# Kernel tuning notes

Hardware: AMD Instinct MI355X
Metric: run time of the kernel (lower is better)

## Reference

```python
import jax, jax.numpy as jnp
import numpy as np

T, N, D, H = 128, 64, 512, 512

def setup_inputs() -> dict:
    key = jax.random.key(0)
    ks = jax.random.split(key, 8)
    x = jax.random.normal(ks[0], (T * N, D), jnp.float32)
    hxs = jax.random.normal(ks[1], (N, H), jnp.float32)
    hxs_1 = jax.random.normal(ks[2], (N, H), jnp.float32)
    masks = jax.random.randint(ks[3], (T * N, 1), 0, 2).astype(jnp.float32)
    w_ih = jax.random.normal(ks[4], (3 * H, D), jnp.float32) / np.sqrt(D).astype(np.float32)
    w_hh = jax.random.normal(ks[5], (3 * H, H), jnp.float32) / np.sqrt(H).astype(np.float32)
    b_ih = jnp.zeros((3 * H,), jnp.float32)
    b_hh = jnp.zeros((3 * H,), jnp.float32)
    return {"x": x, "hxs": hxs, "hxs_1": hxs_1, "masks": masks,
            "w_ih": w_ih, "w_hh": w_hh, "b_ih": b_ih, "b_hh": b_hh}


def _masked_gru(x, hxs, masks, w_ih, w_hh, b_ih, b_hh):
    # Fused equivalent of the torch segment-splitting loop: the torch code
    # resets the hidden state (h * mask) at every step where any mask is 0;
    # within a segment all masks are 1, so applying h * mask_t every step is
    # exactly equivalent, with no host sync / dynamic splitting.
    n = hxs.shape[0]
    h_dim = hxs.shape[1]
    t = x.shape[0] // n
    xt = x.reshape(t, n, -1)            # [T, N, D]
    mt = masks.reshape(t, n, 1)         # [T, N, 1]
    # Precompute all input projections in one big GEMM: [T, N, 3H]
    gi = jnp.einsum('tnd,gd->tng', xt, w_ih) + b_ih

    def step(h, inp):
        gi_t, m_t = inp
        h = h * m_t                      # per-step mask reset
        gh = h @ w_hh.T + b_hh           # [N, 3H]
        i_r, i_z, i_n = jnp.split(gi_t, 3, axis=-1)
        h_r, h_z, h_n = jnp.split(gh, 3, axis=-1)
        r = jax.nn.sigmoid(i_r + h_r)
        z = jax.nn.sigmoid(i_z + h_z)
        ncand = jnp.tanh(i_n + r * h_n)
        h_new = (1.0 - z) * ncand + z * h
        return h_new, h_new

    h_last, outs = jax.lax.scan(step, hxs, (gi, mt))
    return outs.reshape(t * n, h_dim), h_last


def reference(x, hxs, hxs_1, masks, w_ih, w_hh, b_ih, b_hh):
    out, h_last = _masked_gru(x, hxs, masks, w_ih, w_hh, b_ih, b_hh)
    return out, h_last, hxs_1
```

## Files before the change

kernel.cpp:

```cpp
#include <hip/hip_runtime.h>
#include <cmath>

#define TT 128
#define NN 64
#define DD 512
#define HH 512
#define GG 1536

#define META_OFF   0
#define BATCH_OFF  1024
#define TASK_OFF   32768
#define WT_OFF     262144
#define GI_OFF     4194304
#define WS_NEEDED  (GI_OFF + (size_t)TT * NN * GG * 4)

__global__ void build_tasks(const float* __restrict__ masks,
                            int* __restrict__ meta,
                            int4* __restrict__ tasks,
                            int4* __restrict__ batches) {
  __shared__ int hist[TT + 1];
  __shared__ int offs[TT + 1];
  const int tid = threadIdx.x;
  for (int i = tid; i <= TT; i += blockDim.x) hist[i] = 0;
  __syncthreads();
  if (tid < NN) {
    const int n = tid;
    int start = 0;
    for (int t = 1; t < TT; ++t) {
      if (masks[t * NN + n] == 0.0f) { atomicAdd(&hist[t - start], 1); start = t; }
    }
    atomicAdd(&hist[TT - start], 1);
  }
  __syncthreads();
  if (tid == 0) {
    int acc = 0;
    for (int l = TT; l >= 1; --l) { offs[l] = acc; acc += hist[l]; }
    meta[0] = acc;
  }
  __syncthreads();
  const int totalTasks = meta[0];
  if (tid < NN) {
    const int n = tid;
    int start = 0;
    for (int t = 1; t < TT; ++t) {
      if (masks[t * NN + n] == 0.0f) {
        const int len = t - start;
        const int pos = atomicAdd(&offs[len], 1);
        const int seeded = (start == 0 && masks[n] != 0.0f) ? 1 : 0;
        tasks[pos] = make_int4(n, start, len, seeded);
        start = t;
      }
    }
    const int len = TT - start;
    const int pos = atomicAdd(&offs[len], 1);
    const int seeded = (start == 0 && masks[n] != 0.0f) ? 1 : 0;
    tasks[pos] = make_int4(n, start, len, seeded);
  }
  __syncthreads();
  if (tid == 0) {
    const int c0end = offs[5];
    const int c1end = offs[3];
    int b = 0;
    for (int p = 0; p < c0end; p += 4) {
      int c = c0end - p; if (c > 4) c = 4;
      batches[b++] = make_int4(p, 4, c, 0);
    }
    for (int p = c0end; p < c1end; p += 8) {
      int c = c1end - p; if (c > 8) c = 8;
      batches[b++] = make_int4(p, 8, c, 0);
    }
    for (int p = c1end; p < totalTasks; p += 16) {
      int c = totalTasks - p; if (c > 16) c = 16;
      batches[b++] = make_int4(p, 16, c, 0);
    }
    meta[2] = b;
    meta[1] = 0;
  }
}

__global__ void transpose_whh(const float* __restrict__ w, float* __restrict__ wT) {
  const int k = blockIdx.y;
  const int r = blockIdx.x * 256 + threadIdx.x;
  wT[k * GG + r] = w[r * DD + k];
}

__global__ __launch_bounds__(256, 4) void gemm_gi(const float* __restrict__ x,
                                                  const float* __restrict__ w,
                                                  const float* __restrict__ bias,
                                                  float* __restrict__ gi) {
  __shared__ __align__(16) float As[32][132];
  __shared__ __align__(16) float Bs[32][132];
  const int tid = threadIdx.x;
  const int m0 = blockIdx.y * 128;
  const int n0 = blockIdx.x * 128;
  const int tx = tid & 15;
  const int ty = tid >> 4;
  float acc[8][8] = {};
  for (int k0 = 0; k0 < DD; k0 += 32) {
#pragma unroll
    for (int i = 0; i < 4; ++i) {
      const int q = tid + i * 256;
      const int row = q >> 3;
      const int kf = (q & 7) << 2;
      const float4 va = *(const float4*)&x[(size_t)(m0 + row) * DD + k0 + kf];
      As[kf + 0][row] = va.x; As[kf + 1][row] = va.y;
      As[kf + 2][row] = va.z; As[kf + 3][row] = va.w;
      const float4 vb = *(const float4*)&w[(size_t)(n0 + row) * DD + k0 + kf];
      Bs[kf + 0][row] = vb.x; Bs[kf + 1][row] = vb.y;
      Bs[kf + 2][row] = vb.z; Bs[kf + 3][row] = vb.w;
    }
    __syncthreads();
#pragma unroll
    for (int k = 0; k < 32; ++k) {
      float a[8], b[8];
      ((float4*)a)[0] = *(const float4*)&As[k][ty * 8];
      ((float4*)a)[1] = *(const float4*)&As[k][ty * 8 + 4];
      ((float4*)b)[0] = *(const float4*)&Bs[k][tx * 8];
      ((float4*)b)[1] = *(const float4*)&Bs[k][tx * 8 + 4];
#pragma unroll
      for (int i = 0; i < 8; ++i)
#pragma unroll
        for (int j = 0; j < 8; ++j) acc[i][j] = fmaf(a[i], b[j], acc[i][j]);
    }
    __syncthreads();
  }
  float bs[8];
  ((float4*)bs)[0] = *(const float4*)&bias[n0 + tx * 8];
  ((float4*)bs)[1] = *(const float4*)&bias[n0 + tx * 8 + 4];
#pragma unroll
  for (int i = 0; i < 8; ++i) {
    const int row = m0 + ty * 8 + i;
    float4 o0 = make_float4(acc[i][0] + bs[0], acc[i][1] + bs[1],
                            acc[i][2] + bs[2], acc[i][3] + bs[3]);
    float4 o1 = make_float4(acc[i][4] + bs[4], acc[i][5] + bs[5],
                            acc[i][6] + bs[6], acc[i][7] + bs[7]);
    *(float4*)&gi[(size_t)row * GG + n0 + tx * 8] = o0;
    *(float4*)&gi[(size_t)row * GG + n0 + tx * 8 + 4] = o1;
  }
}

template <int W>
__device__ __forceinline__ void process_batch(
    const float* __restrict__ gi, const float* __restrict__ wT,
    const float* __restrict__ hxs, const float* __restrict__ masks,
    float* __restrict__ out, float (*Hs)[16], const int4* s_task, int tid,
    float bh_r, float bh_z, float bh_n) {
  int t_n[W], t_t0[W], t_len[W];
  bool anySeed = false;
#pragma unroll
  for (int c = 0; c < W; ++c) {
    const int4 tk = s_task[c];
    t_n[c] = tk.x; t_t0[c] = tk.y; t_len[c] = tk.z;
    anySeed |= (tk.w != 0 && tk.z > 0);
  }
  const int maxlen = t_len[0];
#pragma unroll
  for (int c = 0; c < W; ++c) {
    float h0 = 0.0f;
    if (s_task[c].w != 0) h0 = masks[t_n[c]] * hxs[t_n[c] * HH + tid];
    Hs[tid][c] = h0;
  }
  __syncthreads();
  for (int s = 0; s < maxlen; ++s) {
    float accr[W], accz[W], accn[W];
#pragma unroll
    for (int c = 0; c < W; ++c) { accr[c] = 0.f; accz[c] = 0.f; accn[c] = 0.f; }
    if (s > 0 || anySeed) {
      const float* w = wT + tid;
#pragma unroll 4
      for (int k = 0; k < HH; ++k) {
        const float wr = w[0];
        const float wz = w[512];
        const float wn = w[1024];
        float hk[W];
        if constexpr (W >= 4)  ((float4*)hk)[0] = *(const float4*)&Hs[k][0];
        if constexpr (W >= 8)  ((float4*)hk)[1] = *(const float4*)&Hs[k][4];
        if constexpr (W >= 16) {
          ((float4*)hk)[2] = *(const float4*)&Hs[k][8];
          ((float4*)hk)[3] = *(const float4*)&Hs[k][12];
        }
#pragma unroll
        for (int c = 0; c < W; ++c) {
          accr[c] = fmaf(wr, hk[c], accr[c]);
          accz[c] = fmaf(wz, hk[c], accz[c]);
          accn[c] = fmaf(wn, hk[c], accn[c]);
        }
        w += GG;
      }
    }
    __syncthreads();
#pragma unroll
    for (int c = 0; c < W; ++c) {
      if (s < t_len[c]) {
        const int row = (t_t0[c] + s) * NN + t_n[c];
        const float* g = gi + (size_t)row * GG + tid;
        const float gr = g[0], gz = g[512], gn = g[1024];
        const float r = 1.0f / (1.0f + expf(-(gr + accr[c] + bh_r)));
        const float z = 1.0f / (1.0f + expf(-(gz + accz[c] + bh_z)));
        const float hold = Hs[tid][c];
        const float nc = tanhf(gn + r * (accn[c] + bh_n));
        const float hnew = (1.0f - z) * nc + z * hold;
        out[(size_t)row * HH + tid] = hnew;
        Hs[tid][c] = hnew;
      }
    }
    __syncthreads();
  }
}

__global__ __launch_bounds__(512, 2) void gru_seq(
    const float* __restrict__ gi, const float* __restrict__ wT,
    const float* __restrict__ b_hh, const float* __restrict__ hxs,
    const float* __restrict__ masks, float* __restrict__ out,
    int* __restrict__ meta, const int4* __restrict__ tasks,
    const int4* __restrict__ batches) {
  __shared__ __align__(16) float Hs[HH][16];
  __shared__ int4 s_task[16];
  __shared__ int s_bidx;
  const int tid = threadIdx.x;
  const float bh_r = b_hh[tid];
  const float bh_z = b_hh[512 + tid];
  const float bh_n = b_hh[1024 + tid];
  const int nBatches = meta[2];
  while (true) {
    if (tid == 0) s_bidx = atomicAdd(&meta[1], 1);
    __syncthreads();
    const int bidx = s_bidx;
    if (bidx >= nBatches) break;
    const int4 bd = batches[bidx];
    if (tid < 16) s_task[tid] = (tid < bd.z) ? tasks[bd.x + tid] : make_int4(0, 0, 0, 0);
    __syncthreads();
    switch (bd.y) {
      case 4:
        process_batch<4>(gi, wT, hxs, masks, out, Hs, s_task, tid, bh_r, bh_z, bh_n);
        break;
      case 8:
        process_batch<8>(gi, wT, hxs, masks, out, Hs, s_task, tid, bh_r, bh_z, bh_n);
        break;
      default:
        process_batch<16>(gi, wT, hxs, masks, out, Hs, s_task, tid, bh_r, bh_z, bh_n);
        break;
    }
  }
}

__global__ void tail_copy(const float4* __restrict__ src_out,
                          const float4* __restrict__ hxs1,
                          float4* __restrict__ dst) {
  const int i = blockIdx.x * 256 + threadIdx.x;
  if (i < 8192)
    dst[1048576 + i] = src_out[1040384 + i];
  else
    dst[1048576 + i] = hxs1[i - 8192];
}

extern "C" void kernel_launch(void* const* d_in, const int* in_sizes, int n_in,
                              void* d_out, int out_size, void* d_ws, size_t ws_size,
                              hipStream_t stream) {
  const float* x      = (const float*)d_in[0];
  const float* hxs    = (const float*)d_in[1];
  const float* hxs_1  = (const float*)d_in[2];
  const float* masks  = (const float*)d_in[3];
  const float* w_ih   = (const float*)d_in[4];
  const float* w_hh   = (const float*)d_in[5];
  const float* b_ih   = (const float*)d_in[6];
  const float* b_hh   = (const float*)d_in[7];
  float* out = (float*)d_out;
  char* ws = (char*)d_ws;
  if (ws_size < WS_NEEDED) return;

  int*  meta    = (int*)(ws + META_OFF);
  int4* batches = (int4*)(ws + BATCH_OFF);
  int4* tasks   = (int4*)(ws + TASK_OFF);
  float* wT     = (float*)(ws + WT_OFF);
  float* gi     = (float*)(ws + GI_OFF);

  build_tasks<<<1, 128, 0, stream>>>(masks, meta, tasks, batches);
  transpose_whh<<<dim3(6, 512), 256, 0, stream>>>(w_hh, wT);
  gemm_gi<<<dim3(12, 64), 256, 0, stream>>>(x, w_ih, b_ih, gi);
  gru_seq<<<256, 512, 0, stream>>>(gi, wT, b_hh, hxs, masks, out, meta, tasks, batches);
  tail_copy<<<64, 256, 0, stream>>>((const float4*)out, (const float4*)hxs_1,
                                    (float4*)out);
}
```

Baseline: 770.6 us.

## Replace per-segment sequential GRU with cooperative depth-round scheduling across the grid

Drops the segment-batch scheduler, in which each block ran whole segments sequentially and reread the transposed W_hh from global memory at every step. Rows are now grouped by depth since the last mask reset. One cooperative kernel processes each depth round across all 256 blocks, with each block holding a 16-column slice of W_hh in shared memory, and grid.sync runs between rounds. Rows where the mask is zero are computed up front without the recurrent matmul. The transpose and tail-copy kernels are folded in, at the cost of one grid-wide barrier per round and a launch that depends on cooperative residency.

```diff
diff --git a/kernel.cpp b/kernel.cpp
--- a/kernel.cpp
+++ b/kernel.cpp
@@ -1,5 +1,8 @@
 #include <hip/hip_runtime.h>
+#include <hip/hip_cooperative_groups.h>
 #include <cmath>
+
+namespace cg = cooperative_groups;
 
 #define TT 128
 #define NN 64
@@ -8,80 +11,67 @@
 #define GG 1536
 
 #define META_OFF   0
-#define BATCH_OFF  1024
-#define TASK_OFF   32768
-#define WT_OFF     262144
-#define GI_OFF     4194304
+#define ROFF_OFF   256
+#define ZROWS_OFF  4096
+#define ROWOUT_OFF 36864
+#define ROWHS_OFF  69632
+#define GI_OFF     1048576
 #define WS_NEEDED  (GI_OFF + (size_t)TT * NN * GG * 4)
 
-__global__ void build_tasks(const float* __restrict__ masks,
-                            int* __restrict__ meta,
-                            int4* __restrict__ tasks,
-                            int4* __restrict__ batches) {
-  __shared__ int hist[TT + 1];
-  __shared__ int offs[TT + 1];
+__global__ void build_rounds(const float* __restrict__ masks, int* __restrict__ meta,
+                             int* __restrict__ roundOff, int* __restrict__ zRows,
+                             int* __restrict__ rowOut, int* __restrict__ rowHsrc) {
+  __shared__ int cnt[129];
+  __shared__ int cur[129];
+  __shared__ int zcur;
   const int tid = threadIdx.x;
-  for (int i = tid; i <= TT; i += blockDim.x) hist[i] = 0;
+  for (int i = tid; i < 129; i += 128) cnt[i] = 0;
+  if (tid == 0) zcur = 0;
   __syncthreads();
   if (tid < NN) {
     const int n = tid;
-    int start = 0;
-    for (int t = 1; t < TT; ++t) {
-      if (masks[t * NN + n] == 0.0f) { atomicAdd(&hist[t - start], 1); start = t; }
-    }
-    atomicAdd(&hist[TT - start], 1);
+    int depth = 0;
+    for (int t = 0; t < TT; ++t) {
+      if (masks[t * NN + n] == 0.0f) {
+        depth = 0;
+        atomicAdd(&zcur, 1);
+      } else {
+        depth = (t == 0) ? 0 : depth + 1;
+        atomicAdd(&cnt[depth], 1);
+      }
+    }
   }
   __syncthreads();
   if (tid == 0) {
-    int acc = 0;
-    for (int l = TT; l >= 1; --l) { offs[l] = acc; acc += hist[l]; }
-    meta[0] = acc;
+    int acc = 0, maxs = -1;
+    for (int s = 0; s < 129; ++s) {
+      roundOff[s] = acc;
+      cur[s] = acc;
+      if (cnt[s] > 0) maxs = s;
+      acc += cnt[s];
+    }
+    roundOff[129] = acc;
+    meta[0] = maxs;
+    meta[1] = zcur;
+    zcur = 0;
   }
   __syncthreads();
-  const int totalTasks = meta[0];
   if (tid < NN) {
     const int n = tid;
-    int start = 0;
-    for (int t = 1; t < TT; ++t) {
+    int depth = 0;
+    for (int t = 0; t < TT; ++t) {
       if (masks[t * NN + n] == 0.0f) {
-        const int len = t - start;
-        const int pos = atomicAdd(&offs[len], 1);
-        const int seeded = (start == 0 && masks[n] != 0.0f) ? 1 : 0;
-        tasks[pos] = make_int4(n, start, len, seeded);
-        start = t;
-      }
-    }
-    const int len = TT - start;
-    const int pos = atomicAdd(&offs[len], 1);
-    const int seeded = (start == 0 && masks[n] != 0.0f) ? 1 : 0;
-    tasks[pos] = make_int4(n, start, len, seeded);
-  }
-  __syncthreads();
-  if (tid == 0) {
-    const int c0end = offs[5];
-    const int c1end = offs[3];
-    int b = 0;
-    for (int p = 0; p < c0end; p += 4) {
-      int c = c0end - p; if (c > 4) c = 4;
-      batches[b++] = make_int4(p, 4, c, 0);
-    }
-    for (int p = c0end; p < c1end; p += 8) {
-      int c = c1end - p; if (c > 8) c = 8;
-      batches[b++] = make_int4(p, 8, c, 0);
-    }
-    for (int p = c1end; p < totalTasks; p += 16) {
-      int c = totalTasks - p; if (c > 16) c = 16;
-      batches[b++] = make_int4(p, 16, c, 0);
-    }
-    meta[2] = b;
-    meta[1] = 0;
-  }
-}
-
-__global__ void transpose_whh(const float* __restrict__ w, float* __restrict__ wT) {
-  const int k = blockIdx.y;
-  const int r = blockIdx.x * 256 + threadIdx.x;
-  wT[k * GG + r] = w[r * DD + k];
+        depth = 0;
+        const int p = atomicAdd(&zcur, 1);
+        zRows[p] = t * NN + n;
+      } else {
+        depth = (t == 0) ? 0 : depth + 1;
+        const int p = atomicAdd(&cur[depth], 1);
+        rowOut[p] = t * NN + n;
+        rowHsrc[p] = (t == 0) ? (8192 + n) : ((t - 1) * NN + n);
+      }
+    }
+  }
 }
 
 __global__ __launch_bounds__(256, 4) void gemm_gi(const float* __restrict__ x,
@@ -139,146 +129,207 @@
   }
 }
 
-template <int W>
-__device__ __forceinline__ void process_batch(
-    const float* __restrict__ gi, const float* __restrict__ wT,
-    const float* __restrict__ hxs, const float* __restrict__ masks,
-    float* __restrict__ out, float (*Hs)[16], const int4* s_task, int tid,
-    float bh_r, float bh_z, float bh_n) {
-  int t_n[W], t_t0[W], t_len[W];
-  bool anySeed = false;
-#pragma unroll
-  for (int c = 0; c < W; ++c) {
-    const int4 tk = s_task[c];
-    t_n[c] = tk.x; t_t0[c] = tk.y; t_len[c] = tk.z;
-    anySeed |= (tk.w != 0 && tk.z > 0);
-  }
-  const int maxlen = t_len[0];
-#pragma unroll
-  for (int c = 0; c < W; ++c) {
-    float h0 = 0.0f;
-    if (s_task[c].w != 0) h0 = masks[t_n[c]] * hxs[t_n[c] * HH + tid];
-    Hs[tid][c] = h0;
-  }
+#define NGC 32
+#define GCW 16
+#define NRG 8
+#define RT  128
+#define KT  32
+#define WSTR 516
+#define HSTR 36
+
+__global__ __launch_bounds__(512) void gru_rounds(
+    const float* __restrict__ gi, const float* __restrict__ w_hh,
+    const float* __restrict__ b_hh, const float* __restrict__ hxs,
+    const float* __restrict__ hxs_1, float* __restrict__ out,
+    const int* __restrict__ meta, const int* __restrict__ roundOff,
+    const int* __restrict__ zRows, const int* __restrict__ rowOut,
+    const int* __restrict__ rowHsrc) {
+  __shared__ __align__(16) float wS[3 * GCW * WSTR];
+  __shared__ __align__(16) float hS[2 * RT * HSTR];
+  __shared__ const float* s_hbase[RT];
+  __shared__ int s_orow[RT];
+
+  const int tid = threadIdx.x;
+  const int bid = blockIdx.x;
+  const int cgrp = bid & (NGC - 1);
+  const int rg = bid >> 5;
+  const int wv = tid >> 6;
+  const int ln = tid & 63;
+  const int tc = ln & 15;
+  const int rsub = ln >> 4;
+  const int lrbase = wv * 16 + rsub * 4;
+  const int col = cgrp * GCW + tc;
+
+  {
+    const float* src = w_hh;
+    for (int q = tid; q < 3 * GCW * 128; q += 512) {
+      const int gr = q >> 7;
+      const int p = q & 127;
+      const int g = gr >> 4, r = gr & 15;
+      const float4 v =
+          *(const float4*)&src[((size_t)(g * 512 + cgrp * GCW + r)) * 512 + p * 4];
+      *(float4*)&wS[(g * GCW + r) * WSTR + p * 4] = v;
+    }
+  }
+  const float bhr = b_hh[col], bhz = b_hh[512 + col], bhn = b_hh[1024 + col];
   __syncthreads();
-  for (int s = 0; s < maxlen; ++s) {
-    float accr[W], accz[W], accn[W];
-#pragma unroll
-    for (int c = 0; c < W; ++c) { accr[c] = 0.f; accz[c] = 0.f; accn[c] = 0.f; }
-    if (s > 0 || anySeed) {
-      const float* w = wT + tid;
-#pragma unroll 4
-      for (int k = 0; k < HH; ++k) {
-        const float wr = w[0];
-        const float wz = w[512];
-        const float wn = w[1024];
-        float hk[W];
-        if constexpr (W >= 4)  ((float4*)hk)[0] = *(const float4*)&Hs[k][0];
-        if constexpr (W >= 8)  ((float4*)hk)[1] = *(const float4*)&Hs[k][4];
-        if constexpr (W >= 16) {
-          ((float4*)hk)[2] = *(const float4*)&Hs[k][8];
-          ((float4*)hk)[3] = *(const float4*)&Hs[k][12];
-        }
-#pragma unroll
-        for (int c = 0; c < W; ++c) {
-          accr[c] = fmaf(wr, hk[c], accr[c]);
-          accz[c] = fmaf(wz, hk[c], accz[c]);
-          accn[c] = fmaf(wn, hk[c], accn[c]);
-        }
-        w += GG;
-      }
-    }
-    __syncthreads();
-#pragma unroll
-    for (int c = 0; c < W; ++c) {
-      if (s < t_len[c]) {
-        const int row = (t_t0[c] + s) * NN + t_n[c];
-        const float* g = gi + (size_t)row * GG + tid;
-        const float gr = g[0], gz = g[512], gn = g[1024];
-        const float r = 1.0f / (1.0f + expf(-(gr + accr[c] + bh_r)));
-        const float z = 1.0f / (1.0f + expf(-(gz + accz[c] + bh_z)));
-        const float hold = Hs[tid][c];
-        const float nc = tanhf(gn + r * (accn[c] + bh_n));
-        const float hnew = (1.0f - z) * nc + z * hold;
-        out[(size_t)row * HH + tid] = hnew;
-        Hs[tid][c] = hnew;
-      }
-    }
-    __syncthreads();
-  }
-}
-
-__global__ __launch_bounds__(512, 2) void gru_seq(
-    const float* __restrict__ gi, const float* __restrict__ wT,
-    const float* __restrict__ b_hh, const float* __restrict__ hxs,
-    const float* __restrict__ masks, float* __restrict__ out,
-    int* __restrict__ meta, const int4* __restrict__ tasks,
-    const int4* __restrict__ batches) {
-  __shared__ __align__(16) float Hs[HH][16];
-  __shared__ int4 s_task[16];
-  __shared__ int s_bidx;
-  const int tid = threadIdx.x;
-  const float bh_r = b_hh[tid];
-  const float bh_z = b_hh[512 + tid];
-  const float bh_n = b_hh[1024 + tid];
-  const int nBatches = meta[2];
-  while (true) {
-    if (tid == 0) s_bidx = atomicAdd(&meta[1], 1);
-    __syncthreads();
-    const int bidx = s_bidx;
-    if (bidx >= nBatches) break;
-    const int4 bd = batches[bidx];
-    if (tid < 16) s_task[tid] = (tid < bd.z) ? tasks[bd.x + tid] : make_int4(0, 0, 0, 0);
-    __syncthreads();
-    switch (bd.y) {
-      case 4:
-        process_batch<4>(gi, wT, hxs, masks, out, Hs, s_task, tid, bh_r, bh_z, bh_n);
-        break;
-      case 8:
-        process_batch<8>(gi, wT, hxs, masks, out, Hs, s_task, tid, bh_r, bh_z, bh_n);
-        break;
-      default:
-        process_batch<16>(gi, wT, hxs, masks, out, Hs, s_task, tid, bh_r, bh_z, bh_n);
-        break;
-    }
-  }
-}
-
-__global__ void tail_copy(const float4* __restrict__ src_out,
-                          const float4* __restrict__ hxs1,
-                          float4* __restrict__ dst) {
-  const int i = blockIdx.x * 256 + threadIdx.x;
-  if (i < 8192)
-    dst[1048576 + i] = src_out[1040384 + i];
-  else
-    dst[1048576 + i] = hxs1[i - 8192];
+
+  cg::grid_group grid = cg::this_grid();
+  const int gtid = bid * 512 + tid;
+  const int gnt = gridDim.x * 512;
+
+  const int zcount = meta[1];
+  for (int idx = gtid; idx < zcount * 512; idx += gnt) {
+    const int zr = zRows[idx >> 9];
+    const int c = idx & 511;
+    const float* g = gi + (size_t)zr * GG + c;
+    const float r = 1.0f / (1.0f + expf(-(g[0] + b_hh[c])));
+    const float z = 1.0f / (1.0f + expf(-(g[512] + b_hh[512 + c])));
+    const float nc = tanhf(g[1024] + r * b_hh[1024 + c]);
+    out[(size_t)zr * HH + c] = (1.0f - z) * nc;
+  }
+
+  const int maxs = meta[0];
+  for (int s = 0; s <= maxs; ++s) {
+    const int base = roundOff[s];
+    const int cnt = roundOff[s + 1] - base;
+    const int chunk = (cnt + NRG - 1) / NRG;
+    const int rowStart = rg * chunk;
+    int myCnt = cnt - rowStart;
+    myCnt = myCnt < 0 ? 0 : (myCnt > chunk ? chunk : myCnt);
+
+    for (int t0 = 0; t0 < myCnt; t0 += RT) {
+      const int rows = min(RT, myCnt - t0);
+      __syncthreads();
+      for (int r = tid; r < RT; r += 512) {
+        if (r < rows) {
+          const int gidx = base + rowStart + t0 + r;
+          s_orow[r] = rowOut[gidx];
+          const int hs = rowHsrc[gidx];
+          s_hbase[r] = (hs >= 8192) ? (hxs + (size_t)(hs - 8192) * HH)
+                                    : (out + (size_t)hs * HH);
+        } else {
+          s_orow[r] = -1;
+          s_hbase[r] = hxs;
+        }
+      }
+      __syncthreads();
+
+      float acc[4][3];
+#pragma unroll
+      for (int j = 0; j < 4; ++j)
+#pragma unroll
+        for (int g2 = 0; g2 < 3; ++g2) acc[j][g2] = 0.0f;
+
+      const int sr0 = tid >> 3, sk0 = (tid & 7) * 4;
+      const int sr1 = (tid + 512) >> 3, sk1 = ((tid + 512) & 7) * 4;
+      float4 st0, st1;
+      st0 = *(const float4*)(s_hbase[sr0] + sk0);
+      st1 = *(const float4*)(s_hbase[sr1] + sk1);
+      *(float4*)&hS[sr0 * HSTR + sk0] = st0;
+      *(float4*)&hS[sr1 * HSTR + sk1] = st1;
+      st0 = *(const float4*)(s_hbase[sr0] + KT + sk0);
+      st1 = *(const float4*)(s_hbase[sr1] + KT + sk1);
+      __syncthreads();
+
+      const bool rowAct = (lrbase < rows);
+      for (int c = 0; c < 16; ++c) {
+        if (rowAct) {
+          const float* hbuf = hS + (c & 1) * RT * HSTR + lrbase * HSTR;
+          const float* wbuf = wS + tc * WSTR + c * KT;
+#pragma unroll
+          for (int kk = 0; kk < KT; kk += 4) {
+            const float4 w0 = *(const float4*)(wbuf + kk);
+            const float4 w1 = *(const float4*)(wbuf + GCW * WSTR + kk);
+            const float4 w2 = *(const float4*)(wbuf + 2 * GCW * WSTR + kk);
+#pragma unroll
+            for (int j = 0; j < 4; ++j) {
+              const float4 hv = *(const float4*)(hbuf + j * HSTR + kk);
+              acc[j][0] = fmaf(w0.x, hv.x, acc[j][0]);
+              acc[j][0] = fmaf(w0.y, hv.y, acc[j][0]);
+              acc[j][0] = fmaf(w0.z, hv.z, acc[j][0]);
+              acc[j][0] = fmaf(w0.w, hv.w, acc[j][0]);
+              acc[j][1] = fmaf(w1.x, hv.x, acc[j][1]);
+              acc[j][1] = fmaf(w1.y, hv.y, acc[j][1]);
+              acc[j][1] = fmaf(w1.z, hv.z, acc[j][1]);
+              acc[j][1] = fmaf(w1.w, hv.w, acc[j][1]);
+              acc[j][2] = fmaf(w2.x, hv.x, acc[j][2]);
+              acc[j][2] = fmaf(w2.y, hv.y, acc[j][2]);
+              acc[j][2] = fmaf(w2.z, hv.z, acc[j][2]);
+              acc[j][2] = fmaf(w2.w, hv.w, acc[j][2]);
+            }
+          }
+        }
+        if (c + 1 < 16) {
+          float* hb = hS + ((c + 1) & 1) * RT * HSTR;
+          *(float4*)&hb[sr0 * HSTR + sk0] = st0;
+          *(float4*)&hb[sr1 * HSTR + sk1] = st1;
+        }
+        if (c + 2 < 16) {
+          st0 = *(const float4*)(s_hbase[sr0] + (c + 2) * KT + sk0);
+          st1 = *(const float4*)(s_hbase[sr1] + (c + 2) * KT + sk1);
+        }
+        __syncthreads();
+      }
+
+#pragma unroll
+      for (int j = 0; j < 4; ++j) {
+        const int lr = lrbase + j;
+        if (lr < rows) {
+          const int orow = s_orow[lr];
+          const float* gp = gi + (size_t)orow * GG + col;
+          const float gr = gp[0], gz = gp[512], gn = gp[1024];
+          const float r = 1.0f / (1.0f + expf(-(gr + acc[j][0] + bhr)));
+          const float z = 1.0f / (1.0f + expf(-(gz + acc[j][1] + bhz)));
+          const float hold = s_hbase[lr][col];
+          const float nc = tanhf(gn + r * (acc[j][2] + bhn));
+          out[(size_t)orow * HH + col] = (1.0f - z) * nc + z * hold;
+        }
+      }
+    }
+    __threadfence();
+    grid.sync();
+  }
+
+  for (int i = gtid; i < 16384; i += gnt) {
+    float4 v;
+    if (i < 8192)
+      v = ((const float4*)out)[1040384 + i];
+    else
+      v = ((const float4*)hxs_1)[i - 8192];
+    ((float4*)out)[1048576 + i] = v;
+  }
 }
 
 extern "C" void kernel_launch(void* const* d_in, const int* in_sizes, int n_in,
                               void* d_out, int out_size, void* d_ws, size_t ws_size,
                               hipStream_t stream) {
-  const float* x      = (const float*)d_in[0];
-  const float* hxs    = (const float*)d_in[1];
-  const float* hxs_1  = (const float*)d_in[2];
-  const float* masks  = (const float*)d_in[3];
-  const float* w_ih   = (const float*)d_in[4];
-  const float* w_hh   = (const float*)d_in[5];
-  const float* b_ih   = (const float*)d_in[6];
-  const float* b_hh   = (const float*)d_in[7];
+  const float* x     = (const float*)d_in[0];
+  const float* hxs   = (const float*)d_in[1];
+  const float* hxs_1 = (const float*)d_in[2];
+  const float* masks = (const float*)d_in[3];
+  const float* w_ih  = (const float*)d_in[4];
+  const float* w_hh  = (const float*)d_in[5];
+  const float* b_ih  = (const float*)d_in[6];
+  const float* b_hh  = (const float*)d_in[7];
   float* out = (float*)d_out;
   char* ws = (char*)d_ws;
   if (ws_size < WS_NEEDED) return;
 
-  int*  meta    = (int*)(ws + META_OFF);
-  int4* batches = (int4*)(ws + BATCH_OFF);
-  int4* tasks   = (int4*)(ws + TASK_OFF);
-  float* wT     = (float*)(ws + WT_OFF);
+  int* meta     = (int*)(ws + META_OFF);
+  int* roundOff = (int*)(ws + ROFF_OFF);
+  int* zRows    = (int*)(ws + ZROWS_OFF);
+  int* rowOut   = (int*)(ws + ROWOUT_OFF);
+  int* rowHsrc  = (int*)(ws + ROWHS_OFF);
   float* gi     = (float*)(ws + GI_OFF);
 
-  build_tasks<<<1, 128, 0, stream>>>(masks, meta, tasks, batches);
-  transpose_whh<<<dim3(6, 512), 256, 0, stream>>>(w_hh, wT);
+  build_rounds<<<1, 128, 0, stream>>>(masks, meta, roundOff, zRows, rowOut, rowHsrc);
   gemm_gi<<<dim3(12, 64), 256, 0, stream>>>(x, w_ih, b_ih, gi);
-  gru_seq<<<256, 512, 0, stream>>>(gi, wT, b_hh, hxs, masks, out, meta, tasks, batches);
-  tail_copy<<<64, 256, 0, stream>>>((const float4*)out, (const float4*)hxs_1,
-                                    (float4*)out);
+
+  const float* gi_c = gi;
+  void* args[] = {(void*)&gi_c,  (void*)&w_hh,    (void*)&b_hh,  (void*)&hxs,
+                  (void*)&hxs_1, (void*)&out,     (void*)&meta,  (void*)&roundOff,
+                  (void*)&zRows, (void*)&rowOut,  (void*)&rowHsrc};
+  hipLaunchCooperativeKernel((const void*)gru_rounds, dim3(256), dim3(512), args, 0,
+                             stream);
 }
```

Result: slower. 1.545 ms (+100.5%).

## Split GRU segments across four column-slice blocks with atomic step sync

Applied to the files above, without the earlier changes.

Segments now start at each mask-zero row. A separate elementwise kernel computes those zero-hidden rows, where the recurrent term vanishes. Each batch of 8 segments is split over 4 workgroups, one per 128-column slice, so each block holds only its slice of w_hh in cache. Blocks exchange the hidden state through global memory and wait on a per-batch atomic counter after every step. This adds parallelism and reduces weight traffic per block, at the cost of a global-memory round trip and a spin-wait each step, plus a risk of deadlock if the blocks for one batch are not co-resident.

```diff
diff --git a/kernel.cpp b/kernel.cpp
--- a/kernel.cpp
+++ b/kernel.cpp
@@ -6,82 +6,76 @@
 #define DD 512
 #define HH 512
 #define GG 1536
-
-#define META_OFF   0
-#define BATCH_OFF  1024
-#define TASK_OFF   32768
-#define WT_OFF     262144
-#define GI_OFF     4194304
-#define WS_NEEDED  (GI_OFF + (size_t)TT * NN * GG * 4)
-
-__global__ void build_tasks(const float* __restrict__ masks,
-                            int* __restrict__ meta,
-                            int4* __restrict__ tasks,
-                            int4* __restrict__ batches) {
-  __shared__ int hist[TT + 1];
-  __shared__ int offs[TT + 1];
+#define WW 8
+#define GQ 4
+
+#define META_OFF 0
+#define CTR_OFF  4096
+#define SEG_OFF  40960
+#define ZR_OFF   131072
+#define GI_OFF   4194304
+#define WS_NEEDED (GI_OFF + (size_t)TT * NN * GG * 4)
+
+__global__ void build_chains(const float* __restrict__ masks, int* __restrict__ meta,
+                             int* __restrict__ ctr, int4* __restrict__ segs,
+                             int* __restrict__ zRows) {
+  __shared__ int hist[129];
+  __shared__ int offs[129];
+  __shared__ int zc;
+  __shared__ int nsegS;
   const int tid = threadIdx.x;
-  for (int i = tid; i <= TT; i += blockDim.x) hist[i] = 0;
+  for (int i = tid; i < 129; i += 128) hist[i] = 0;
+  for (int i = tid; i < 512 * 16; i += 128) ctr[i] = 0;
+  if (tid == 0) zc = 0;
   __syncthreads();
   if (tid < NN) {
     const int n = tid;
-    int start = 0;
-    for (int t = 1; t < TT; ++t) {
-      if (masks[t * NN + n] == 0.0f) { atomicAdd(&hist[t - start], 1); start = t; }
-    }
-    atomicAdd(&hist[TT - start], 1);
+    int run = 0;
+    for (int t = 0; t < TT; ++t) {
+      const bool m = masks[t * NN + n] != 0.0f;
+      if (m) ++run;
+      if (!m) {
+        atomicAdd(&zc, 1);
+        if (run > 0) { atomicAdd(&hist[run], 1); run = 0; }
+      } else if (t == TT - 1) {
+        atomicAdd(&hist[run], 1);
+      }
+    }
   }
   __syncthreads();
   if (tid == 0) {
     int acc = 0;
-    for (int l = TT; l >= 1; --l) { offs[l] = acc; acc += hist[l]; }
-    meta[0] = acc;
+    for (int l = 128; l >= 1; --l) { offs[l] = acc; acc += hist[l]; }
+    nsegS = acc;
+    meta[2] = zc;
+    zc = 0;
   }
   __syncthreads();
-  const int totalTasks = meta[0];
   if (tid < NN) {
     const int n = tid;
-    int start = 0;
-    for (int t = 1; t < TT; ++t) {
-      if (masks[t * NN + n] == 0.0f) {
-        const int len = t - start;
-        const int pos = atomicAdd(&offs[len], 1);
-        const int seeded = (start == 0 && masks[n] != 0.0f) ? 1 : 0;
-        tasks[pos] = make_int4(n, start, len, seeded);
-        start = t;
-      }
-    }
-    const int len = TT - start;
-    const int pos = atomicAdd(&offs[len], 1);
-    const int seeded = (start == 0 && masks[n] != 0.0f) ? 1 : 0;
-    tasks[pos] = make_int4(n, start, len, seeded);
+    int run = 0, tf = 0;
+    for (int t = 0; t < TT; ++t) {
+      const bool m = masks[t * NN + n] != 0.0f;
+      if (m) { if (run == 0) tf = t; ++run; }
+      if (!m) {
+        const int p = atomicAdd(&zc, 1);
+        zRows[p] = t * NN + n;
+        if (run > 0) {
+          const int pp = atomicAdd(&offs[run], 1);
+          segs[pp] = make_int4(n, tf, run, 0);
+          run = 0;
+        }
+      } else if (t == TT - 1) {
+        const int pp = atomicAdd(&offs[run], 1);
+        segs[pp] = make_int4(n, tf, run, 0);
+      }
+    }
   }
   __syncthreads();
-  if (tid == 0) {
-    const int c0end = offs[5];
-    const int c1end = offs[3];
-    int b = 0;
-    for (int p = 0; p < c0end; p += 4) {
-      int c = c0end - p; if (c > 4) c = 4;
-      batches[b++] = make_int4(p, 4, c, 0);
-    }
-    for (int p = c0end; p < c1end; p += 8) {
-      int c = c1end - p; if (c > 8) c = 8;
-      batches[b++] = make_int4(p, 8, c, 0);
-    }
-    for (int p = c1end; p < totalTasks; p += 16) {
-      int c = totalTasks - p; if (c > 16) c = 16;
-      batches[b++] = make_int4(p, 16, c, 0);
-    }
-    meta[2] = b;
-    meta[1] = 0;
-  }
-}
-
-__global__ void transpose_whh(const float* __restrict__ w, float* __restrict__ wT) {
-  const int k = blockIdx.y;
-  const int r = blockIdx.x * 256 + threadIdx.x;
-  wT[k * GG + r] = w[r * DD + k];
+  const int nseg = nsegS;
+  const int nB = (nseg + WW - 1) / WW;
+  for (int i = nseg + tid; i < nB * WW; i += 128) segs[i] = make_int4(0, 1, 0, 0);
+  if (tid == 0) { meta[0] = 0; meta[1] = nB * GQ; meta[3] = nB; }
 }
 
 __global__ __launch_bounds__(256, 4) void gemm_gi(const float* __restrict__ x,
@@ -139,107 +133,142 @@
   }
 }
 
-template <int W>
-__device__ __forceinline__ void process_batch(
-    const float* __restrict__ gi, const float* __restrict__ wT,
-    const float* __restrict__ hxs, const float* __restrict__ masks,
-    float* __restrict__ out, float (*Hs)[16], const int4* s_task, int tid,
-    float bh_r, float bh_z, float bh_n) {
-  int t_n[W], t_t0[W], t_len[W];
-  bool anySeed = false;
-#pragma unroll
-  for (int c = 0; c < W; ++c) {
-    const int4 tk = s_task[c];
-    t_n[c] = tk.x; t_t0[c] = tk.y; t_len[c] = tk.z;
-    anySeed |= (tk.w != 0 && tk.z > 0);
-  }
-  const int maxlen = t_len[0];
-#pragma unroll
-  for (int c = 0; c < W; ++c) {
-    float h0 = 0.0f;
-    if (s_task[c].w != 0) h0 = masks[t_n[c]] * hxs[t_n[c] * HH + tid];
-    Hs[tid][c] = h0;
-  }
-  __syncthreads();
-  for (int s = 0; s < maxlen; ++s) {
-    float accr[W], accz[W], accn[W];
-#pragma unroll
-    for (int c = 0; c < W; ++c) { accr[c] = 0.f; accz[c] = 0.f; accn[c] = 0.f; }
-    if (s > 0 || anySeed) {
-      const float* w = wT + tid;
-#pragma unroll 4
-      for (int k = 0; k < HH; ++k) {
-        const float wr = w[0];
-        const float wz = w[512];
-        const float wn = w[1024];
-        float hk[W];
-        if constexpr (W >= 4)  ((float4*)hk)[0] = *(const float4*)&Hs[k][0];
-        if constexpr (W >= 8)  ((float4*)hk)[1] = *(const float4*)&Hs[k][4];
-        if constexpr (W >= 16) {
-          ((float4*)hk)[2] = *(const float4*)&Hs[k][8];
-          ((float4*)hk)[3] = *(const float4*)&Hs[k][12];
+__global__ void heads_ew(const float* __restrict__ gi, const float* __restrict__ b_hh,
+                         const int* __restrict__ meta, const int* __restrict__ zRows,
+                         float* __restrict__ out) {
+  const int total = meta[2] * HH;
+  for (int idx = blockIdx.x * blockDim.x + threadIdx.x; idx < total;
+       idx += gridDim.x * blockDim.x) {
+    const int zr = zRows[idx >> 9];
+    const int c = idx & 511;
+    const float* g = gi + (size_t)zr * GG + c;
+    const float r = 1.0f / (1.0f + expf(-(g[0] + b_hh[c])));
+    const float z = 1.0f / (1.0f + expf(-(g[512] + b_hh[512 + c])));
+    const float nc = tanhf(g[1024] + r * b_hh[1024 + c]);
+    out[(size_t)zr * HH + c] = (1.0f - z) * nc;
+  }
+}
+
+__global__ __launch_bounds__(512) void gru_chains(
+    const float* __restrict__ gi, const float* __restrict__ w_hh,
+    const float* __restrict__ b_hh, const float* __restrict__ hxs,
+    float* __restrict__ out, int* __restrict__ meta, int* __restrict__ ctr,
+    const int4* __restrict__ segs) {
+  __shared__ __align__(16) float hS[WW][520];
+  __shared__ __align__(16) float red[3 * WW][516];
+  __shared__ int4 sseg[WW];
+  __shared__ int sTask;
+
+  const int tid = threadIdx.x;
+  const int cc = tid & 127;
+  const int q = tid >> 7;
+  const int nTasks = meta[1];
+
+  while (true) {
+    if (tid == 0) sTask = atomicAdd(&meta[0], 1);
+    __syncthreads();
+    const int task = sTask;
+    if (task >= nTasks) break;
+    const int b = task >> 2;
+    const int gq = task & 3;
+    const int cb = gq * 128;
+    if (tid < WW) sseg[tid] = segs[b * WW + tid];
+    __syncthreads();
+    const int maxlen = sseg[0].z;
+    const int col = cb + cc;
+    const float bhr = b_hh[col];
+    const float bhz = b_hh[512 + col];
+    const float bhn = b_hh[1024 + col];
+    const float* w0 = w_hh + (size_t)(col) * DD + q * 128;
+    const float* w1 = w_hh + (size_t)(512 + col) * DD + q * 128;
+    const float* w2 = w_hh + (size_t)(1024 + col) * DD + q * 128;
+
+    for (int s = 0; s < maxlen; ++s) {
+      if (s > 0) {
+        if (tid == 0) {
+          while (__hip_atomic_load(&ctr[b * 16], __ATOMIC_ACQUIRE,
+                                   __HIP_MEMORY_SCOPE_AGENT) < GQ * s) {}
         }
-#pragma unroll
-        for (int c = 0; c < W; ++c) {
-          accr[c] = fmaf(wr, hk[c], accr[c]);
-          accz[c] = fmaf(wz, hk[c], accz[c]);
-          accn[c] = fmaf(wn, hk[c], accn[c]);
+        __syncthreads();
+        __threadfence();
+      }
+      {
+        const int j = tid >> 6, l = tid & 63;
+        const int4 sg = sseg[j];
+        const int r = sg.y - 1 + s;
+        const bool act = (s < sg.z);
+        const float* hp = act ? ((r >= 0) ? out + (size_t)(r * NN + sg.x) * HH
+                                          : hxs + (size_t)sg.x * HH)
+                              : out;
+        const float4 v0 = *(const float4*)(hp + l * 8);
+        const float4 v1 = *(const float4*)(hp + l * 8 + 4);
+        *(float4*)&hS[j][l * 8] = v0;
+        *(float4*)&hS[j][l * 8 + 4] = v1;
+      }
+      __syncthreads();
+
+      float acc0[WW], acc1[WW], acc2[WW];
+#pragma unroll
+      for (int j = 0; j < WW; ++j) { acc0[j] = 0.f; acc1[j] = 0.f; acc2[j] = 0.f; }
+#pragma unroll 2
+      for (int k = 0; k < 128; k += 4) {
+        const float4 a0 = *(const float4*)(w0 + k);
+        const float4 a1 = *(const float4*)(w1 + k);
+        const float4 a2 = *(const float4*)(w2 + k);
+#pragma unroll
+        for (int j = 0; j < WW; ++j) {
+          const float4 hv = *(const float4*)&hS[j][q * 128 + k];
+          acc0[j] = fmaf(a0.x, hv.x, acc0[j]);
+          acc0[j] = fmaf(a0.y, hv.y, acc0[j]);
+          acc0[j] = fmaf(a0.z, hv.z, acc0[j]);
+          acc0[j] = fmaf(a0.w, hv.w, acc0[j]);
+          acc1[j] = fmaf(a1.x, hv.x, acc1[j]);
+          acc1[j] = fmaf(a1.y, hv.y, acc1[j]);
+          acc1[j] = fmaf(a1.z, hv.z, acc1[j]);
+          acc1[j] = fmaf(a1.w, hv.w, acc1[j]);
+          acc2[j] = fmaf(a2.x, hv.x, acc2[j]);
+          acc2[j] = fmaf(a2.y, hv.y, acc2[j]);
+          acc2[j] = fmaf(a2.z, hv.z, acc2[j]);
+          acc2[j] = fmaf(a2.w, hv.w, acc2[j]);
         }
-        w += GG;
-      }
-    }
-    __syncthreads();
-#pragma unroll
-    for (int c = 0; c < W; ++c) {
-      if (s < t_len[c]) {
-        const int row = (t_t0[c] + s) * NN + t_n[c];
-        const float* g = gi + (size_t)row * GG + tid;
-        const float gr = g[0], gz = g[512], gn = g[1024];
-        const float r = 1.0f / (1.0f + expf(-(gr + accr[c] + bh_r)));
-        const float z = 1.0f / (1.0f + expf(-(gz + accz[c] + bh_z)));
-        const float hold = Hs[tid][c];
-        const float nc = tanhf(gn + r * (accn[c] + bh_n));
-        const float hnew = (1.0f - z) * nc + z * hold;
-        out[(size_t)row * HH + tid] = hnew;
-        Hs[tid][c] = hnew;
-      }
-    }
-    __syncthreads();
-  }
-}
-
-__global__ __launch_bounds__(512, 2) void gru_seq(
-    const float* __restrict__ gi, const float* __restrict__ wT,
-    const float* __restrict__ b_hh, const float* __restrict__ hxs,
-    const float* __restrict__ masks, float* __restrict__ out,
-    int* __restrict__ meta, const int4* __restrict__ tasks,
-    const int4* __restrict__ batches) {
-  __shared__ __align__(16) float Hs[HH][16];
-  __shared__ int4 s_task[16];
-  __shared__ int s_bidx;
-  const int tid = threadIdx.x;
-  const float bh_r = b_hh[tid];
-  const float bh_z = b_hh[512 + tid];
-  const float bh_n = b_hh[1024 + tid];
-  const int nBatches = meta[2];
-  while (true) {
-    if (tid == 0) s_bidx = atomicAdd(&meta[1], 1);
-    __syncthreads();
-    const int bidx = s_bidx;
-    if (bidx >= nBatches) break;
-    const int4 bd = batches[bidx];
-    if (tid < 16) s_task[tid] = (tid < bd.z) ? tasks[bd.x + tid] : make_int4(0, 0, 0, 0);
-    __syncthreads();
-    switch (bd.y) {
-      case 4:
-        process_batch<4>(gi, wT, hxs, masks, out, Hs, s_task, tid, bh_r, bh_z, bh_n);
-        break;
-      case 8:
-        process_batch<8>(gi, wT, hxs, masks, out, Hs, s_task, tid, bh_r, bh_z, bh_n);
-        break;
-      default:
-        process_batch<16>(gi, wT, hxs, masks, out, Hs, s_task, tid, bh_r, bh_z, bh_n);
-        break;
+      }
+#pragma unroll
+      for (int j = 0; j < WW; ++j) {
+        red[0 * WW + j][cc * 4 + q] = acc0[j];
+        red[1 * WW + j][cc * 4 + q] = acc1[j];
+        red[2 * WW + j][cc * 4 + q] = acc2[j];
+      }
+      __syncthreads();
+
+      {
+        const int jp = tid >> 7;
+#pragma unroll
+        for (int e = 0; e < 2; ++e) {
+          const int j = jp * 2 + e;
+          const int4 sg = sseg[j];
+          if (s < sg.z) {
+            const float4 pr = *(const float4*)&red[0 * WW + j][cc * 4];
+            const float4 pz = *(const float4*)&red[1 * WW + j][cc * 4];
+            const float4 pn = *(const float4*)&red[2 * WW + j][cc * 4];
+            const float sr = pr.x + pr.y + pr.z + pr.w;
+            const float sz = pz.x + pz.y + pz.z + pz.w;
+            const float sn = pn.x + pn.y + pn.z + pn.w;
+            const int orow = (sg.y + s) * NN + sg.x;
+            const float* gp = gi + (size_t)orow * GG + col;
+            const float ir = gp[0], iz = gp[512], inn = gp[1024];
+            const float r = 1.0f / (1.0f + expf(-(ir + sr + bhr)));
+            const float z = 1.0f / (1.0f + expf(-(iz + sz + bhz)));
+            const float hold = hS[j][col];
+            const float nc = tanhf(inn + r * (sn + bhn));
+            out[(size_t)orow * HH + col] = (1.0f - z) * nc + z * hold;
+          }
+        }
+      }
+      __threadfence();
+      __syncthreads();
+      if (tid == 0)
+        __hip_atomic_fetch_add(&ctr[b * 16], 1, __ATOMIC_RELEASE,
+                               __HIP_MEMORY_SCOPE_AGENT);
     }
   }
 }
@@ -257,28 +286,28 @@
 extern "C" void kernel_launch(void* const* d_in, const int* in_sizes, int n_in,
                               void* d_out, int out_size, void* d_ws, size_t ws_size,
                               hipStream_t stream) {
-  const float* x      = (const float*)d_in[0];
-  const float* hxs    = (const float*)d_in[1];
-  const float* hxs_1  = (const float*)d_in[2];
-  const float* masks  = (const float*)d_in[3];
-  const float* w_ih   = (const float*)d_in[4];
-  const float* w_hh   = (const float*)d_in[5];
-  const float* b_ih   = (const float*)d_in[6];
-  const float* b_hh   = (const float*)d_in[7];
+  const float* x     = (const float*)d_in[0];
+  const float* hxs   = (const float*)d_in[1];
+  const float* hxs_1 = (const float*)d_in[2];
+  const float* masks = (const float*)d_in[3];
+  const float* w_ih  = (const float*)d_in[4];
+  const float* w_hh  = (const float*)d_in[5];
+  const float* b_ih  = (const float*)d_in[6];
+  const float* b_hh  = (const float*)d_in[7];
   float* out = (float*)d_out;
   char* ws = (char*)d_ws;
   if (ws_size < WS_NEEDED) return;
 
-  int*  meta    = (int*)(ws + META_OFF);
-  int4* batches = (int4*)(ws + BATCH_OFF);
-  int4* tasks   = (int4*)(ws + TASK_OFF);
-  float* wT     = (float*)(ws + WT_OFF);
-  float* gi     = (float*)(ws + GI_OFF);
-
-  build_tasks<<<1, 128, 0, stream>>>(masks, meta, tasks, batches);
-  transpose_whh<<<dim3(6, 512), 256, 0, stream>>>(w_hh, wT);
+  int* meta   = (int*)(ws + META_OFF);
+  int* ctr    = (int*)(ws + CTR_OFF);
+  int4* segs  = (int4*)(ws + SEG_OFF);
+  int* zRows  = (int*)(ws + ZR_OFF);
+  float* gi   = (float*)(ws + GI_OFF);
+
+  build_chains<<<1, 128, 0, stream>>>(masks, meta, ctr, segs, zRows);
   gemm_gi<<<dim3(12, 64), 256, 0, stream>>>(x, w_ih, b_ih, gi);
-  gru_seq<<<256, 512, 0, stream>>>(gi, wT, b_hh, hxs, masks, out, meta, tasks, batches);
+  heads_ew<<<2048, 256, 0, stream>>>(gi, b_hh, meta, zRows, out);
+  gru_chains<<<256, 512, 0, stream>>>(gi, w_hh, b_hh, hxs, out, meta, ctr, segs);
   tail_copy<<<64, 256, 0, stream>>>((const float4*)out, (const float4*)hxs_1,
                                     (float4*)out);
 }
```

After: 1.130 ms. 46.6% more time.
